# Optimization experiments

Hardware: AMD Instinct MI355X
Metric: run time of the kernel (lower is better)

Reference implementation:

```python
import jax, jax.numpy as jnp
import numpy as np

B = 8
N_PER = 8192   # xyz points per batch
M_PER = 2048   # query points per batch
C_FEAT = 32
RADIUS = 0.2
K = 32         # sample_nums
USE_XYZ = True


def setup_inputs() -> dict:
    key = jax.random.key(0)
    k1, k2, k3 = jax.random.split(key, 3)
    xyz = jax.random.uniform(k1, (B * N_PER, 3), dtype=jnp.float32)
    new_xyz = jax.random.uniform(k2, (B * M_PER, 3), dtype=jnp.float32)
    features = jax.random.normal(k3, (B * N_PER, C_FEAT), dtype=jnp.float32)
    xyz_batch_cnt = jnp.full((B,), N_PER, dtype=jnp.int32)
    new_xyz_batch_cnt = jnp.full((B,), M_PER, dtype=jnp.int32)
    return {
        "xyz": xyz,
        "xyz_batch_cnt": xyz_batch_cnt,
        "new_xyz": new_xyz,
        "new_xyz_batch_cnt": new_xyz_batch_cnt,
        "features": features,
    }


def _ball_query(xyz_b, new_b, radius, k):
    # xyz_b: (B, N, 3), new_b: (B, M, 3)
    n = xyz_b.shape[1]
    # squared pairwise distances (B, M, N)
    d2 = jnp.sum((new_b[:, :, None, :] - xyz_b[:, None, :, :]) ** 2, axis=-1)
    mask = d2 < (radius * radius)
    # first-k in-radius indices (CUDA ball_query keeps neighbors in point order)
    scores = jnp.where(mask, jnp.arange(n, dtype=jnp.int32), jnp.int32(n))
    idx_sorted = jnp.sort(scores, axis=-1)[..., :k]          # (B, M, k)
    cnt = jnp.sum(mask, axis=-1)                              # (B, M)
    empty = cnt == 0                                          # (B, M)
    first = idx_sorted[..., :1]                               # duplicate first hit
    slot = jnp.arange(k, dtype=jnp.int32)
    idx = jnp.where(slot[None, None, :] < cnt[..., None], idx_sorted, first)
    idx = jnp.where(empty[..., None], jnp.int32(0), idx)      # empty balls -> 0
    return idx, empty


def reference(xyz, xyz_batch_cnt, new_xyz, new_xyz_batch_cnt, features):
    b = xyz_batch_cnt.shape[0]
    xyz_b = xyz.reshape(b, -1, 3)          # (B, N, 3)
    new_b = new_xyz.reshape(b, -1, 3)      # (B, M, 3)
    feat_b = features.reshape(b, xyz_b.shape[1], -1)  # (B, N, C)

    idx, empty = _ball_query(xyz_b, new_b, RADIUS, K)  # (B, M, K), (B, M)

    gather = jax.vmap(lambda pts, i: pts[i])           # per-batch gather
    grouped_xyz = gather(xyz_b, idx) - new_b[:, :, None, :]   # (B, M, K, 3)
    grouped_xyz = jnp.where(empty[..., None, None], 0.0, grouped_xyz)

    grouped_feat = gather(feat_b, idx)                        # (B, M, K, C)
    grouped_feat = jnp.where(empty[..., None, None], 0.0, grouped_feat)

    if USE_XYZ:
        new_features = jnp.concatenate([grouped_xyz, grouped_feat], axis=-1)
    else:
        new_features = grouped_feat
    # (B, M, K, 3+C) -> (B*M, 3+C, K) to match torch (Mtot, C', nsample)
    m_tot = b * new_b.shape[1]
    new_features = jnp.transpose(new_features, (0, 1, 3, 2)).reshape(
        m_tot, -1, K)
    idx_flat = idx.reshape(m_tot, K)
    return new_features, idx_flat
```

## Files before the change

### kernel.cpp

```cpp
#include <hip/hip_runtime.h>

#define BATCHES   8
#define N_PER     8192
#define M_PER     2048
#define C_FEAT    32
#define KNN       32
#define R2        0.04f
#define M_TOT     (BATCHES * M_PER)
#define FEAT_OUT  (3 + C_FEAT)
#define OUT_FEAT_SZ ((size_t)M_TOT * FEAT_OUT * KNN)

__global__ __launch_bounds__(256) void sqag_fused_kernel(
    const float* __restrict__ xyz,
    const float* __restrict__ new_xyz,
    const float* __restrict__ features,
    float* __restrict__ out)
{
    __shared__ int sidx[4][KNN];

    const int wave = threadIdx.x >> 6;
    const int lane = threadIdx.x & 63;
    const int q    = __builtin_amdgcn_readfirstlane(blockIdx.x * 4 + wave);
    const int b    = q >> 11;
    const int base = b * N_PER;

    const float px = new_xyz[q * 3 + 0];
    const float py = new_xyz[q * 3 + 1];
    const float pz = new_xyz[q * 3 + 2];

    int cnt = 0;
    int first = 0;

    const float* p = xyz + (size_t)base * 3 + lane * 3;
    float x0 = p[0],   y0 = p[1],   z0 = p[2];
    float x1 = p[192], y1 = p[193], z1 = p[194];

    for (int cb = 0;;) {
        const bool more = (cb + 128) < N_PER;
        const float* pn = p + 384;
        float ax0 = 0.f, ay0 = 0.f, az0 = 0.f, ax1 = 0.f, ay1 = 0.f, az1 = 0.f;
        if (more) {
            ax0 = pn[0];   ay0 = pn[1];   az0 = pn[2];
            ax1 = pn[192]; ay1 = pn[193]; az1 = pn[194];
        }

        const float dx0 = px - x0, dy0 = py - y0, dz0 = pz - z0;
        const float dx1 = px - x1, dy1 = py - y1, dz1 = pz - z1;
        const float d20 = __fadd_rn(__fadd_rn(__fmul_rn(dx0, dx0),
                                              __fmul_rn(dy0, dy0)),
                                    __fmul_rn(dz0, dz0));
        const float d21 = __fadd_rn(__fadd_rn(__fmul_rn(dx1, dx1),
                                              __fmul_rn(dy1, dy1)),
                                    __fmul_rn(dz1, dz1));
        const unsigned long long m0 = __ballot(d20 < R2);
        const unsigned long long m1 = __ballot(d21 < R2);

        if (cnt == 0) {
            if (m0)      first = cb + (__ffsll((long long)m0) - 1);
            else if (m1) first = cb + 64 + (__ffsll((long long)m1) - 1);
        }
        const int c0 = __popcll(m0);
        {
            const unsigned r0 = __builtin_amdgcn_mbcnt_hi(
                (unsigned)(m0 >> 32),
                __builtin_amdgcn_mbcnt_lo((unsigned)m0, 0u));
            const unsigned r1 = __builtin_amdgcn_mbcnt_hi(
                (unsigned)(m1 >> 32),
                __builtin_amdgcn_mbcnt_lo((unsigned)m1, 0u));
            if (d20 < R2) {
                const int r = cnt + (int)r0;
                if (r < KNN) sidx[wave][r] = cb + lane;
            }
            if (d21 < R2) {
                const int r = cnt + c0 + (int)r1;
                if (r < KNN) sidx[wave][r] = cb + 64 + lane;
            }
        }
        cnt += c0 + __popcll(m1);

        if (cnt >= KNN || !more) break;
        p = pn;
        cb += 128;
        x0 = ax0; y0 = ay0; z0 = az0;
        x1 = ax1; y1 = ay1; z1 = az1;
    }

    const int pad = (cnt == 0) ? 0 : first;
    if (lane >= cnt && lane < KNN) sidx[wave][lane] = pad;
    const float zf = (cnt == 0) ? 0.0f : 1.0f;

    const int k    = lane & 31;
    const int half = lane >> 5;

    const int li = sidx[wave][k];
    const int gi = base + li;

    const float4* f = (const float4*)(features + (size_t)gi * C_FEAT + half * 16);
    const float4 v0 = f[0];
    const float4 v1 = f[1];
    const float4 v2 = f[2];
    const float4 v3 = f[3];

    const float gx = xyz[(size_t)gi * 3 + 0] - px;
    const float gy = xyz[(size_t)gi * 3 + 1] - py;
    const float gz = xyz[(size_t)gi * 3 + 2] - pz;

    float* o = out + (size_t)q * (FEAT_OUT * KNN);
    if (half == 0) {
        o[0 * KNN + k] = zf * gx;
        o[1 * KNN + k] = zf * gy;
        o[2 * KNN + k] = zf * gz;
        out[OUT_FEAT_SZ + (size_t)q * KNN + k] = (float)li;
    }

    const int jb = 3 + half * 16;
    o[(jb +  0) * KNN + k] = zf * v0.x;
    o[(jb +  1) * KNN + k] = zf * v0.y;
    o[(jb +  2) * KNN + k] = zf * v0.z;
    o[(jb +  3) * KNN + k] = zf * v0.w;
    o[(jb +  4) * KNN + k] = zf * v1.x;
    o[(jb +  5) * KNN + k] = zf * v1.y;
    o[(jb +  6) * KNN + k] = zf * v1.z;
    o[(jb +  7) * KNN + k] = zf * v1.w;
    o[(jb +  8) * KNN + k] = zf * v2.x;
    o[(jb +  9) * KNN + k] = zf * v2.y;
    o[(jb + 10) * KNN + k] = zf * v2.z;
    o[(jb + 11) * KNN + k] = zf * v2.w;
    o[(jb + 12) * KNN + k] = zf * v3.x;
    o[(jb + 13) * KNN + k] = zf * v3.y;
    o[(jb + 14) * KNN + k] = zf * v3.z;
    o[(jb + 15) * KNN + k] = zf * v3.w;
}

extern "C" void kernel_launch(void* const* d_in, const int* in_sizes, int n_in,
                              void* d_out, int out_size, void* d_ws, size_t ws_size,
                              hipStream_t stream) {
    const float* xyz      = (const float*)d_in[0];
    const float* new_xyz  = (const float*)d_in[2];
    const float* features = (const float*)d_in[4];
    float* out = (float*)d_out;

    sqag_fused_kernel<<<M_TOT / 4, 256, 0, stream>>>(xyz, new_xyz, features, out);
}
```

Measured before the change: 134.4 us.

## Widen ball-query scan to 256 points, swizzle blocks across batches, use nontemporal stores

After: 115.6 us. 14.0% less time.

```diff
diff --git a/kernel.cpp b/kernel.cpp
--- a/kernel.cpp
+++ b/kernel.cpp
@@ -20,7 +20,11 @@
 
     const int wave = threadIdx.x >> 6;
     const int lane = threadIdx.x & 63;
-    const int q    = __builtin_amdgcn_readfirstlane(blockIdx.x * 4 + wave);
+
+    const int bswz   = blockIdx.x & 7;
+    const int within = blockIdx.x >> 3;
+    const int q = __builtin_amdgcn_readfirstlane(
+        (bswz * (M_PER / 4) + within) * 4 + wave);
     const int b    = q >> 11;
     const int base = b * N_PER;
 
@@ -31,58 +35,69 @@
     int cnt = 0;
     int first = 0;
 
+    float cx[4], cy[4], cz[4];
     const float* p = xyz + (size_t)base * 3 + lane * 3;
-    float x0 = p[0],   y0 = p[1],   z0 = p[2];
-    float x1 = p[192], y1 = p[193], z1 = p[194];
+    #pragma unroll
+    for (int c = 0; c < 4; ++c) {
+        cx[c] = p[c * 192 + 0];
+        cy[c] = p[c * 192 + 1];
+        cz[c] = p[c * 192 + 2];
+    }
 
     for (int cb = 0;;) {
-        const bool more = (cb + 128) < N_PER;
-        const float* pn = p + 384;
-        float ax0 = 0.f, ay0 = 0.f, az0 = 0.f, ax1 = 0.f, ay1 = 0.f, az1 = 0.f;
+        const bool more = (cb + 256) < N_PER;
+        float nx[4], ny[4], nz[4];
         if (more) {
-            ax0 = pn[0];   ay0 = pn[1];   az0 = pn[2];
-            ax1 = pn[192]; ay1 = pn[193]; az1 = pn[194];
+            const float* pn = p + 768;
+            #pragma unroll
+            for (int c = 0; c < 4; ++c) {
+                nx[c] = pn[c * 192 + 0];
+                ny[c] = pn[c * 192 + 1];
+                nz[c] = pn[c * 192 + 2];
+            }
         }
 
-        const float dx0 = px - x0, dy0 = py - y0, dz0 = pz - z0;
-        const float dx1 = px - x1, dy1 = py - y1, dz1 = pz - z1;
-        const float d20 = __fadd_rn(__fadd_rn(__fmul_rn(dx0, dx0),
-                                              __fmul_rn(dy0, dy0)),
-                                    __fmul_rn(dz0, dz0));
-        const float d21 = __fadd_rn(__fadd_rn(__fmul_rn(dx1, dx1),
-                                              __fmul_rn(dy1, dy1)),
-                                    __fmul_rn(dz1, dz1));
-        const unsigned long long m0 = __ballot(d20 < R2);
-        const unsigned long long m1 = __ballot(d21 < R2);
+        unsigned long long m[4];
+        bool in[4];
+        #pragma unroll
+        for (int c = 0; c < 4; ++c) {
+            const float dx = px - cx[c];
+            const float dy = py - cy[c];
+            const float dz = pz - cz[c];
+            const float d2 = __fadd_rn(__fadd_rn(__fmul_rn(dx, dx),
+                                                 __fmul_rn(dy, dy)),
+                                       __fmul_rn(dz, dz));
+            in[c] = d2 < R2;
+            m[c]  = __ballot(in[c]);
+        }
 
         if (cnt == 0) {
-            if (m0)      first = cb + (__ffsll((long long)m0) - 1);
-            else if (m1) first = cb + 64 + (__ffsll((long long)m1) - 1);
+            if      (m[0]) first = cb +       (__ffsll((long long)m[0]) - 1);
+            else if (m[1]) first = cb +  64 + (__ffsll((long long)m[1]) - 1);
+            else if (m[2]) first = cb + 128 + (__ffsll((long long)m[2]) - 1);
+            else if (m[3]) first = cb + 192 + (__ffsll((long long)m[3]) - 1);
         }
-        const int c0 = __popcll(m0);
-        {
-            const unsigned r0 = __builtin_amdgcn_mbcnt_hi(
-                (unsigned)(m0 >> 32),
-                __builtin_amdgcn_mbcnt_lo((unsigned)m0, 0u));
-            const unsigned r1 = __builtin_amdgcn_mbcnt_hi(
-                (unsigned)(m1 >> 32),
-                __builtin_amdgcn_mbcnt_lo((unsigned)m1, 0u));
-            if (d20 < R2) {
-                const int r = cnt + (int)r0;
-                if (r < KNN) sidx[wave][r] = cb + lane;
+
+        int pre = cnt;
+        #pragma unroll
+        for (int c = 0; c < 4; ++c) {
+            if (in[c]) {
+                const int r = pre + (int)__builtin_amdgcn_mbcnt_hi(
+                    (unsigned)(m[c] >> 32),
+                    __builtin_amdgcn_mbcnt_lo((unsigned)m[c], 0u));
+                if (r < KNN) sidx[wave][r] = cb + c * 64 + lane;
             }
-            if (d21 < R2) {
-                const int r = cnt + c0 + (int)r1;
-                if (r < KNN) sidx[wave][r] = cb + 64 + lane;
-            }
+            pre += __popcll(m[c]);
         }
-        cnt += c0 + __popcll(m1);
+        cnt = pre;
 
         if (cnt >= KNN || !more) break;
-        p = pn;
-        cb += 128;
-        x0 = ax0; y0 = ay0; z0 = az0;
-        x1 = ax1; y1 = ay1; z1 = az1;
+        p += 768;
+        cb += 256;
+        #pragma unroll
+        for (int c = 0; c < 4; ++c) {
+            cx[c] = nx[c]; cy[c] = ny[c]; cz[c] = nz[c];
+        }
     }
 
     const int pad = (cnt == 0) ? 0 : first;
@@ -107,29 +122,30 @@
 
     float* o = out + (size_t)q * (FEAT_OUT * KNN);
     if (half == 0) {
-        o[0 * KNN + k] = zf * gx;
-        o[1 * KNN + k] = zf * gy;
-        o[2 * KNN + k] = zf * gz;
-        out[OUT_FEAT_SZ + (size_t)q * KNN + k] = (float)li;
+        __builtin_nontemporal_store(zf * gx, &o[0 * KNN + k]);
+        __builtin_nontemporal_store(zf * gy, &o[1 * KNN + k]);
+        __builtin_nontemporal_store(zf * gz, &o[2 * KNN + k]);
+        __builtin_nontemporal_store((float)li,
+                                    &out[OUT_FEAT_SZ + (size_t)q * KNN + k]);
     }
 
     const int jb = 3 + half * 16;
-    o[(jb +  0) * KNN + k] = zf * v0.x;
-    o[(jb +  1) * KNN + k] = zf * v0.y;
-    o[(jb +  2) * KNN + k] = zf * v0.z;
-    o[(jb +  3) * KNN + k] = zf * v0.w;
-    o[(jb +  4) * KNN + k] = zf * v1.x;
-    o[(jb +  5) * KNN + k] = zf * v1.y;
-    o[(jb +  6) * KNN + k] = zf * v1.z;
-    o[(jb +  7) * KNN + k] = zf * v1.w;
-    o[(jb +  8) * KNN + k] = zf * v2.x;
-    o[(jb +  9) * KNN + k] = zf * v2.y;
-    o[(jb + 10) * KNN + k] = zf * v2.z;
-    o[(jb + 11) * KNN + k] = zf * v2.w;
-    o[(jb + 12) * KNN + k] = zf * v3.x;
-    o[(jb + 13) * KNN + k] = zf * v3.y;
-    o[(jb + 14) * KNN + k] = zf * v3.z;
-    o[(jb + 15) * KNN + k] = zf * v3.w;
+    __builtin_nontemporal_store(zf * v0.x, &o[(jb +  0) * KNN + k]);
+    __builtin_nontemporal_store(zf * v0.y, &o[(jb +  1) * KNN + k]);
+    __builtin_nontemporal_store(zf * v0.z, &o[(jb +  2) * KNN + k]);
+    __builtin_nontemporal_store(zf * v0.w, &o[(jb +  3) * KNN + k]);
+    __builtin_nontemporal_store(zf * v1.x, &o[(jb +  4) * KNN + k]);
+    __builtin_nontemporal_store(zf * v1.y, &o[(jb +  5) * KNN + k]);
+    __builtin_nontemporal_store(zf * v1.z, &o[(jb +  6) * KNN + k]);
+    __builtin_nontemporal_store(zf * v1.w, &o[(jb +  7) * KNN + k]);
+    __builtin_nontemporal_store(zf * v2.x, &o[(jb +  8) * KNN + k]);
+    __builtin_nontemporal_store(zf * v2.y, &o[(jb +  9) * KNN + k]);
+    __builtin_nontemporal_store(zf * v2.z, &o[(jb + 10) * KNN + k]);
+    __builtin_nontemporal_store(zf * v2.w, &o[(jb + 11) * KNN + k]);
+    __builtin_nontemporal_store(zf * v3.x, &o[(jb + 12) * KNN + k]);
+    __builtin_nontemporal_store(zf * v3.y, &o[(jb + 13) * KNN + k]);
+    __builtin_nontemporal_store(zf * v3.z, &o[(jb + 14) * KNN + k]);
+    __builtin_nontemporal_store(zf * v3.w, &o[(jb + 15) * KNN + k]);
 }
 
 extern "C" void kernel_launch(void* const* d_in, const int* in_sizes, int n_in,
```
